# Performance work log

Measured on AMD Instinct MI355X. Metric: run time of the kernel, lower is better.

Reference implementation:

```python
import jax, jax.numpy as jnp
import numpy as np

B, L, D = 8, 2048, 2048
NH, HD = 32, 64          # num_heads, head_dim (D = NH*HD)
CS = 16                  # inner_net_chunk_size
BASE_LR = 1.0            # inner-loop base learning rate
EPS = 1e-6
ROPE_BASE = 10000.0


def setup_inputs() -> dict:
    key = jax.random.key(0)
    ks = jax.random.split(key, 6)
    s = 0.02
    return {
        "hidden_states": jax.random.normal(ks[0], (B, L, D), jnp.float32),
        "wq": jax.random.normal(ks[1], (D, D), jnp.float32) * s,
        "wk": jax.random.normal(ks[2], (D, D), jnp.float32) * s,
        "wv": jax.random.normal(ks[3], (D, D), jnp.float32) * s,
        "wo": jax.random.normal(ks[4], (D, D), jnp.float32) * s,
        "W1": jax.random.normal(ks[5], (NH, HD, HD), jnp.float32) * s,
        "b1": jnp.zeros((NH, 1, HD), jnp.float32),
        "ttt_norm_weight": jnp.ones((NH, HD), jnp.float32),
        "ttt_norm_bias": jnp.zeros((NH, HD), jnp.float32),
    }


def _rotate_half(x):
    x1, x2 = jnp.split(x, 2, axis=-1)
    return jnp.concatenate((-x2, x1), axis=-1)


def _permute_qk(x):
    b, h, l, f = x.shape
    return x.reshape(b, h, l, f // 2, 2).transpose(0, 1, 2, 4, 3).reshape(b, h, l, f)


def _undo_permute_qk(x):
    b, h, l, f = x.shape
    return x.reshape(b, h, l, 2, f // 2).transpose(0, 1, 2, 4, 3).reshape(b, h, l, f)


def _ln_fwd(x, g, b):
    mu = x.mean(-1, keepdims=True)
    var = ((x - mu) ** 2).mean(-1, keepdims=True)
    xh = (x - mu) * jax.lax.rsqrt(var + EPS)
    return g * xh + b


def _ln_fused_l2_bwd(x, target, g, b):
    # grad of 0.5*||LN(x) - target||^2 w.r.t. x, fused (TTT inner-loop loss grad)
    f = x.shape[-1]
    mu = x.mean(-1, keepdims=True)
    var = ((x - mu) ** 2).mean(-1, keepdims=True)
    std = jnp.sqrt(var + EPS)
    xh = (x - mu) / std
    gout = (g * xh + b) - target
    gxh = gout * g
    return (f * gxh - gxh.sum(-1, keepdims=True)
            - xh * (gxh * xh).sum(-1, keepdims=True)) / (f * std)


def reference(hidden_states, wq, wk, wv, wo, W1, b1, ttt_norm_weight, ttt_norm_bias):
    Bx, Lx, Dx = hidden_states.shape
    nc = Lx // CS

    def proj(w):  # [B,L,D] -> [B,NH,L,HD]
        return (hidden_states @ w).reshape(Bx, Lx, NH, HD).transpose(0, 2, 1, 3)

    XQ, XK, XV = proj(wq), proj(wk), proj(wv)

    # rotary embedding (with permute/undo as in the source)
    inv_freq = 1.0 / (ROPE_BASE ** (jnp.arange(0, HD, 2, dtype=jnp.float32) / HD))
    freqs = jnp.outer(jnp.arange(Lx, dtype=jnp.float32), inv_freq)
    emb = jnp.concatenate((freqs, freqs), axis=-1)
    cos, sin = jnp.cos(emb)[None, None], jnp.sin(emb)[None, None]
    XQ, XK = _permute_qk(XQ), _permute_qk(XK)
    XQ = XQ * cos + _rotate_half(XQ) * sin
    XK = XK * cos + _rotate_half(XK) * sin
    XQ, XK = _undo_permute_qk(XQ), _undo_permute_qk(XK)

    def chunk(x):  # [B,NH,L,HD] -> [nc,B,NH,CS,HD]
        return x.reshape(Bx, NH, nc, CS, HD).transpose(2, 0, 1, 3, 4)

    XQc, XKc, XVc = chunk(XQ), chunk(XK), chunk(XV)

    g = ttt_norm_weight[None, :, None, :]   # [1,NH,1,HD]
    bb = ttt_norm_bias[None, :, None, :]

    token_idx = 1.0 / jnp.arange(1, CS + 1, dtype=jnp.float32)   # buffer from __init__
    eta = BASE_LR * token_idx                                    # [CS]
    tril_eta = jnp.tril(jnp.ones((CS, CS), jnp.float32)) * eta[:, None]
    last_eta = eta[-1]

    W1_0 = jnp.broadcast_to(W1[None], (Bx, NH, HD, HD))
    b1_0 = jnp.broadcast_to(b1[None], (Bx, NH, 1, HD))

    def step(carry, xs):
        W1s, b1s = carry
        xq, xk, xv = xs                                          # [B,NH,CS,HD]
        Z1 = jnp.einsum('bhkf,bhfg->bhkg', xk, W1s) + b1s
        grad = _ln_fused_l2_bwd(Z1, xv - xk, g, bb)              # dl/dZ1
        attn = jnp.tril(jnp.einsum('bhkf,bhlf->bhkl', xq, xk))   # causal within chunk
        b1_bar = b1s - jnp.einsum('kl,bhlf->bhkf', tril_eta, grad)
        Z1_bar = (jnp.einsum('bhkf,bhfg->bhkg', xq, W1s)
                  - jnp.einsum('bhkl,bhlf->bhkf', eta[None, None, :, None] * attn, grad)
                  + b1_bar)
        W1_new = W1s - last_eta * jnp.einsum('bhkf,bhkg->bhfg', xk, grad)
        b1_new = b1s - last_eta * grad.sum(-2, keepdims=True)
        out = xq + _ln_fwd(Z1_bar, g, bb)                        # residual + post-LN
        return (W1_new, b1_new), out

    _, outs = jax.lax.scan(step, (W1_0, b1_0), (XQc, XKc, XVc))  # [nc,B,NH,CS,HD]
    out = (outs.transpose(1, 2, 0, 3, 4).reshape(Bx, NH, Lx, HD)
               .transpose(0, 2, 1, 3).reshape(Bx, Lx, Dx))
    return out @ wo
```

## Files before the change

### kernel.cpp

```cpp
#include <hip/hip_runtime.h>

typedef __bf16 bf16;
typedef __bf16 bf16x4 __attribute__((ext_vector_type(4)));
typedef __bf16 bf16x8 __attribute__((ext_vector_type(8)));
typedef float floatx4 __attribute__((ext_vector_type(4)));

#define BB 8
#define LL 2048
#define DD 2048
#define NHH 32
#define HDD 64

#define MFMA16(a, b, c) __builtin_amdgcn_mfma_f32_16x16x32_bf16(a, b, c, 0, 0, 0)

__device__ __forceinline__ void gl_lds16(const void* g, void* l) {
  __builtin_amdgcn_global_load_lds((const __attribute__((address_space(1))) void*)g,
                                   (__attribute__((address_space(3))) void*)l, 16, 0, 0);
}

__global__ __launch_bounds__(256) void cast_bf16(const float* __restrict__ src,
                                                 bf16* __restrict__ dst)
{
  size_t i = ((size_t)blockIdx.x * 256 + threadIdx.x) * 8;
  floatx4 a = *(const floatx4*)(src + i);
  floatx4 b = *(const floatx4*)(src + i + 4);
  bf16x8 v;
  v[0] = (bf16)a[0]; v[1] = (bf16)a[1]; v[2] = (bf16)a[2]; v[3] = (bf16)a[3];
  v[4] = (bf16)b[0]; v[5] = (bf16)b[1]; v[6] = (bf16)b[2]; v[7] = (bf16)b[3];
  *(bf16x8*)(dst + i) = v;
}

__global__ __launch_bounds__(256) void transpose1(const float* __restrict__ src,
                                                  bf16* __restrict__ dst)
{
  __shared__ float tile[64][65];
  const int t = threadIdx.x;
  const int col = t & 63, rw = t >> 6;
  const int bx = blockIdx.x * 64, by = blockIdx.y * 64;
  for (int i = rw; i < 64; i += 4)
    tile[i][col] = src[(size_t)(by + i) * DD + bx + col];
  __syncthreads();
  for (int i = rw; i < 64; i += 4)
    dst[(size_t)(bx + i) * DD + by + col] = (bf16)tile[col][i];
}

template<int AIDX, int EPI>
__global__ __launch_bounds__(256) void gemm_bt(const bf16* __restrict__ Ab,
    const bf16* __restrict__ BT, void* __restrict__ Cv)
{
  constexpr int Kd = 2048;
  __shared__ alignas(16) bf16 As[128 * 64];
  __shared__ alignas(16) bf16 Bs[128 * 64];
  const int t = threadIdx.x;
  const int id = blockIdx.y * 16 + blockIdx.x;
  const int swz = (id & 7) * 256 + (id >> 3);
  const int bn = swz & 15, bm = swz >> 4;
  const int wave = t >> 6, lane = t & 63;
  const int m16 = lane & 15, quad = lane >> 4;
  floatx4 acc[2][8] = {};
  const int r0 = t >> 3;
  const int scc = (t & 7) ^ (r0 & 7);
  const bf16* Bb = BT + (size_t)(bn * 128) * Kd;
  char* AsB = (char*)As + wave * 1024;
  char* BsB = (char*)Bs + wave * 1024;

  for (int k0 = 0; k0 < Kd; k0 += 64) {
    for (int i = 0; i < 4; ++i) {
      int r = r0 + 32 * i;
      int col = k0 + scc * 8;
      const bf16* ga;
      if (AIDX == 0) {
        ga = Ab + (size_t)(bm * 128 + r) * Kd + col;
      } else {
        int R = bm * 128 + r;
        int b = R >> 11, l = R & 2047;
        int h = col >> 6, f = col & 63;
        ga = Ab + (((size_t)(b * NHH + h) * LL + l) * HDD + f);
      }
      gl_lds16(ga, AsB + i * 4096);
      gl_lds16(Bb + (size_t)r * Kd + col, BsB + i * 4096);
    }
    __syncthreads();
    const int sw = m16 & 7;
    for (int kk = 0; kk < 2; ++kk) {
      bf16x8 af[2], bfr[8];
      const int c = ((kk * 4 + quad) ^ sw) * 8;
      for (int mt = 0; mt < 2; ++mt)
        af[mt] = *(const bf16x8*)&As[(wave * 32 + mt * 16 + m16) * 64 + c];
      for (int nt = 0; nt < 8; ++nt)
        bfr[nt] = *(const bf16x8*)&Bs[(nt * 16 + m16) * 64 + c];
      for (int mt = 0; mt < 2; ++mt)
        for (int nt = 0; nt < 8; ++nt)
          acc[mt][nt] = MFMA16(af[mt], bfr[nt], acc[mt][nt]);
    }
    __syncthreads();
  }

  for (int mt = 0; mt < 2; ++mt)
    for (int nt = 0; nt < 8; ++nt)
      for (int rg = 0; rg < 4; ++rg) {
        int row = bm * 128 + wave * 32 + mt * 16 + quad * 4 + rg;
        int col = bn * 128 + nt * 16 + m16;
        if (EPI == 0) {
          ((float*)Cv)[(size_t)row * DD + col] = acc[mt][nt][rg];
        } else {
          int b = row >> 11, l = row & 2047;
          int h = col >> 6, f = col & 63;
          ((bf16*)Cv)[((size_t)(b * NHH + h) * LL + l) * HDD + f] = (bf16)acc[mt][nt][rg];
        }
      }
}

__global__ __launch_bounds__(256) void rope_qk(bf16* __restrict__ Q, bf16* __restrict__ Kt)
{
  bf16* X = blockIdx.y ? Kt : Q;
  unsigned p = blockIdx.x * 256u + threadIdx.x;
  int i = p & 31;
  int l = (p >> 5) & 2047;
  int bh = p >> 16;
  float invf = expf(-(float)i * 0.28782313662425573f);
  float th = (float)l * invf;
  float cs = cosf(th), sn = sinf(th);
  size_t off = (size_t)bh * (LL * HDD) + (size_t)l * HDD + 2 * i;
  float x0 = (float)X[off], x1 = (float)X[off + 1];
  X[off]     = (bf16)(x0 * cs - x1 * sn);
  X[off + 1] = (bf16)(x1 * cs + x0 * sn);
}

__global__ __launch_bounds__(256) void ttt_scan(
    const bf16* Q, const bf16* __restrict__ Kx,
    const bf16* __restrict__ V, const float* __restrict__ W1g,
    const float* __restrict__ b1g, const float* __restrict__ gw,
    const float* __restrict__ gb, bf16* O)
{
  const int bh = blockIdx.x, h = bh & 31;
  const int t = threadIdx.x;
  const int wave = t >> 6, lane = t & 63;
  const int q = lane >> 4, i16 = lane & 15;
  const int kr = t >> 4, sr = t & 15, f0 = sr * 4;

  __shared__ alignas(16) bf16 W1Th[64 * 72];
  __shared__ alignas(16) bf16 W1Tl[64 * 72];
  __shared__ alignas(16) bf16 xqs[2][16 * 72];
  __shared__ alignas(16) bf16 xks[2][16 * 72];
  __shared__ alignas(16) bf16 xvs[2][16 * 72];
  __shared__ alignas(16) bf16 xkTs[64 * 24];
  __shared__ alignas(16) bf16 gTh[64 * 24];
  __shared__ alignas(16) bf16 gTl[64 * 24];
  __shared__ alignas(16) bf16 Pm[16 * 24];
  __shared__ alignas(16) float Z1s[16 * 68];

  floatx4 accW[4];
  const float* Wg = W1g + (size_t)h * 4096;
  for (int mt = 0; mt < 4; ++mt)
    for (int r = 0; r < 4; ++r)
      accW[mt][r] = Wg[(16 * mt + 4 * q + r) * 64 + 16 * wave + i16];
  float b1r = b1g[h * 64 + 16 * wave + i16];

  for (int mt = 0; mt < 4; ++mt) {
    bf16x4 h4, l4;
    for (int r = 0; r < 4; ++r) {
      float w = accW[mt][r];
      bf16 hi = (bf16)w;
      h4[r] = hi; l4[r] = (bf16)(w - (float)hi);
    }
    int base = (16 * wave + i16) * 72 + 16 * mt + 4 * q;
    *(bf16x4*)&W1Th[base] = h4;
    *(bf16x4*)&W1Tl[base] = l4;
  }

  float gq[4], bq[4];
  for (int j = 0; j < 4; ++j) {
    gq[j] = gw[h * 64 + f0 + j];
    bq[j] = gb[h * 64 + f0 + j];
  }
  float etar[4];
  for (int r = 0; r < 4; ++r) etar[r] = 1.0f / (float)(4 * q + r + 1);

  const size_t qbase = (size_t)bh * (LL * HDD);
  bf16x4 rq = *(const bf16x4*)(Q  + qbase + kr * 64 + f0);
  bf16x4 rk = *(const bf16x4*)(Kx + qbase + kr * 64 + f0);
  bf16x4 rv = *(const bf16x4*)(V  + qbase + kr * 64 + f0);

  for (int c = 0; c < 128; ++c) {
    const int pb = c & 1;
    *(bf16x4*)&xqs[pb][kr * 72 + f0] = rq;
    *(bf16x4*)&xks[pb][kr * 72 + f0] = rk;
    *(bf16x4*)&xvs[pb][kr * 72 + f0] = rv;
    for (int j = 0; j < 4; ++j)
      xkTs[(f0 + j) * 24 + kr] = (bf16)((float)rk[j] * -0.0625f);
    __syncthreads();

    bf16x8 akf[2], whi[2], wlo[2];
    akf[0] = *(const bf16x8*)&xks[pb][i16 * 72 + q * 8];
    akf[1] = *(const bf16x8*)&xks[pb][i16 * 72 + 32 + q * 8];
    {
      int wb = (16 * wave + i16) * 72 + q * 8;
      whi[0] = *(const bf16x8*)&W1Th[wb];
      whi[1] = *(const bf16x8*)&W1Th[wb + 32];
      wlo[0] = *(const bf16x8*)&W1Tl[wb];
      wlo[1] = *(const bf16x8*)&W1Tl[wb + 32];
    }
    {
      floatx4 z = {b1r, b1r, b1r, b1r};
      z = MFMA16(akf[0], whi[0], z);
      z = MFMA16(akf[1], whi[1], z);
      z = MFMA16(akf[0], wlo[0], z);
      z = MFMA16(akf[1], wlo[1], z);
      for (int r = 0; r < 4; ++r)
        Z1s[(4 * q + r) * 68 + 16 * wave + i16] = z[r];
    }
    if (wave == 0) {
      bf16x8 aq0 = *(const bf16x8*)&xqs[pb][i16 * 72 + q * 8];
      bf16x8 aq1 = *(const bf16x8*)&xqs[pb][i16 * 72 + 32 + q * 8];
      floatx4 at = {};
      at = MFMA16(aq0, akf[0], at);
      at = MFMA16(aq1, akf[1], at);
      for (int r = 0; r < 4; ++r) {
        int krow = 4 * q + r;
        float pv = (i16 <= krow) ? -(at[r] + 1.0f) * etar[r] : 0.0f;
        Pm[krow * 24 + i16] = (bf16)pv;
      }
    }
    __syncthreads();

    {
      floatx4 z4 = *(const floatx4*)&Z1s[kr * 68 + f0];
      float tg[4], sum = 0.f, ssq = 0.f;
      for (int j = 0; j < 4; ++j) {
        tg[j] = (float)rv[j] - (float)rk[j];
        sum += z4[j]; ssq += z4[j] * z4[j];
      }
      for (int m = 1; m < 16; m <<= 1) { sum += __shfl_xor(sum, m, 64); ssq += __shfl_xor(ssq, m, 64); }
      float mu = sum * (1.f / 64.f);
      float var = ssq * (1.f / 64.f) - mu * mu;
      float rstd = rsqrtf(var + 1e-6f);
      float xh[4], gx[4], s1 = 0.f, s2 = 0.f;
      for (int j = 0; j < 4; ++j) {
        xh[j] = (z4[j] - mu) * rstd;
        float go = gq[j] * xh[j] + bq[j] - tg[j];
        gx[j] = go * gq[j];
        s1 += gx[j]; s2 += gx[j] * xh[j];
      }
      for (int m = 1; m < 16; m <<= 1) { s1 += __shfl_xor(s1, m, 64); s2 += __shfl_xor(s2, m, 64); }
      for (int j = 0; j < 4; ++j) {
        float gr = (64.f * gx[j] - s1 - xh[j] * s2) * (rstd * (1.f / 64.f));
        bf16 hi = (bf16)gr;
        gTh[(f0 + j) * 24 + kr] = hi;
        gTl[(f0 + j) * 24 + kr] = (bf16)(gr - (float)hi);
      }
    }
    __syncthreads();

    {
      const size_t cb = qbase + (size_t)(c + 1) * 1024 + kr * 64 + f0;
      rq = *(const bf16x4*)(Q  + cb);
      rk = *(const bf16x4*)(Kx + cb);
      rv = *(const bf16x4*)(V  + cb);
    }

    {
      bf16x8 aq0 = *(const bf16x8*)&xqs[pb][i16 * 72 + q * 8];
      bf16x8 aq1 = *(const bf16x8*)&xqs[pb][i16 * 72 + 32 + q * 8];
      bf16x8 pf  = *(const bf16x8*)&Pm[i16 * 24 + (q & 1) * 8];
      const bf16* gT = (q < 2) ? gTh : gTl;
      bf16x8 bgp = *(const bf16x8*)&gT[(16 * wave + i16) * 24 + (q & 1) * 8];
      floatx4 zb = {b1r, b1r, b1r, b1r};
      zb = MFMA16(aq0, whi[0], zb);
      zb = MFMA16(aq1, whi[1], zb);
      zb = MFMA16(aq0, wlo[0], zb);
      zb = MFMA16(aq1, wlo[1], zb);
      zb = MFMA16(pf, bgp, zb);
      for (int r = 0; r < 4; ++r)
        Z1s[(4 * q + r) * 68 + 16 * wave + i16] = zb[r];

      for (int mt = 0; mt < 4; ++mt) {
        bf16x8 axk = *(const bf16x8*)&xkTs[(16 * mt + i16) * 24 + (q & 1) * 8];
        accW[mt] = MFMA16(axk, bgp, accW[mt]);
      }
      for (int mt = 0; mt < 4; ++mt) {
        bf16x4 h4, l4;
        for (int r = 0; r < 4; ++r) {
          float w = accW[mt][r];
          bf16 hi = (bf16)w;
          h4[r] = hi; l4[r] = (bf16)(w - (float)hi);
        }
        int base = (16 * wave + i16) * 72 + 16 * mt + 4 * q;
        *(bf16x4*)&W1Th[base] = h4;
        *(bf16x4*)&W1Tl[base] = l4;
      }
      {
        const bf16* rh = &gTh[(16 * wave + i16) * 24];
        const bf16* rl = &gTl[(16 * wave + i16) * 24];
        bf16x8 a0 = *(const bf16x8*)rh, a1 = *(const bf16x8*)(rh + 8);
        bf16x8 a2 = *(const bf16x8*)rl, a3 = *(const bf16x8*)(rl + 8);
        float s = 0.f;
        for (int j = 0; j < 8; ++j)
          s += (float)a0[j] + (float)a1[j] + (float)a2[j] + (float)a3[j];
        b1r -= 0.0625f * s;
      }
    }
    __syncthreads();

    {
      floatx4 z4 = *(const floatx4*)&Z1s[kr * 68 + f0];
      float sum = 0.f, ssq = 0.f;
      for (int j = 0; j < 4; ++j) { sum += z4[j]; ssq += z4[j] * z4[j]; }
      for (int m = 1; m < 16; m <<= 1) { sum += __shfl_xor(sum, m, 64); ssq += __shfl_xor(ssq, m, 64); }
      float mu = sum * (1.f / 64.f);
      float var = ssq * (1.f / 64.f) - mu * mu;
      float rstd = rsqrtf(var + 1e-6f);
      bf16x4 xq4 = *(const bf16x4*)&xqs[pb][kr * 72 + f0];
      bf16x4 o4;
      for (int j = 0; j < 4; ++j)
        o4[j] = (bf16)((float)xq4[j] + gq[j] * ((z4[j] - mu) * rstd) + bq[j]);
      *(bf16x4*)(O + qbase + (size_t)c * 1024 + kr * 64 + f0) = o4;
    }
  }
}

extern "C" void kernel_launch(void* const* d_in, const int* in_sizes, int n_in,
                              void* d_out, int out_size, void* d_ws, size_t ws_size,
                              hipStream_t stream)
{
  const float* X  = (const float*)d_in[0];
  const float* wq = (const float*)d_in[1];
  const float* wk = (const float*)d_in[2];
  const float* wv = (const float*)d_in[3];
  const float* wo = (const float*)d_in[4];
  const float* W1 = (const float*)d_in[5];
  const float* b1 = (const float*)d_in[6];
  const float* gw = (const float*)d_in[7];
  const float* gb = (const float*)d_in[8];

  bf16* ws = (bf16*)d_ws;
  const size_t NEl = (size_t)BB * LL * DD;
  bf16* Qb = ws;
  bf16* Kb = ws + NEl;
  bf16* WT = ws + 2 * NEl;
  bf16* Vb = (bf16*)d_out;
  bf16* Xb = (bf16*)d_out + NEl;

  cast_bf16<<<dim3(16384), 256, 0, stream>>>(X, Xb);
  transpose1<<<dim3(32, 32), 256, 0, stream>>>(wq, WT);
  gemm_bt<0, 1><<<dim3(16, 128), 256, 0, stream>>>(Xb, WT, Qb);
  transpose1<<<dim3(32, 32), 256, 0, stream>>>(wk, WT);
  gemm_bt<0, 1><<<dim3(16, 128), 256, 0, stream>>>(Xb, WT, Kb);
  transpose1<<<dim3(32, 32), 256, 0, stream>>>(wv, WT);
  gemm_bt<0, 1><<<dim3(16, 128), 256, 0, stream>>>(Xb, WT, Vb);
  rope_qk<<<dim3(65536, 2), 256, 0, stream>>>(Qb, Kb);
  ttt_scan<<<dim3(256), 256, 0, stream>>>(Qb, Kb, Vb, W1, b1, gw, gb, Qb);
  transpose1<<<dim3(32, 32), 256, 0, stream>>>(wo, WT);
  gemm_bt<1, 0><<<dim3(16, 128), 256, 0, stream>>>(Qb, WT, d_out);
}
```

Measured before the change: 1.209 ms.

## Pipeline GEMM with triple-buffered LDS, 256x128 tiles and 8 waves

Result: slower. 1.313 ms (+8.6%).

```diff
diff --git a/kernel.cpp b/kernel.cpp
--- a/kernel.cpp
+++ b/kernel.cpp
@@ -45,62 +45,100 @@
 }
 
 template<int AIDX, int EPI>
-__global__ __launch_bounds__(256) void gemm_bt(const bf16* __restrict__ Ab,
+__global__ __launch_bounds__(512) void gemm_bt(const bf16* __restrict__ Ab,
     const bf16* __restrict__ BT, void* __restrict__ Cv)
 {
   constexpr int Kd = 2048;
-  __shared__ alignas(16) bf16 As[128 * 64];
-  __shared__ alignas(16) bf16 Bs[128 * 64];
+  constexpr int NT = Kd / 64;
+  __shared__ alignas(16) bf16 As[3][256 * 64];
+  __shared__ alignas(16) bf16 Bs[3][128 * 64];
   const int t = threadIdx.x;
   const int id = blockIdx.y * 16 + blockIdx.x;
-  const int swz = (id & 7) * 256 + (id >> 3);
+  const int swz = (id & 7) * 128 + (id >> 3);
   const int bn = swz & 15, bm = swz >> 4;
-  const int wave = t >> 6, lane = t & 63;
-  const int m16 = lane & 15, quad = lane >> 4;
-  floatx4 acc[2][8] = {};
-  const int r0 = t >> 3;
-  const int scc = (t & 7) ^ (r0 & 7);
-  const bf16* Bb = BT + (size_t)(bn * 128) * Kd;
-  char* AsB = (char*)As + wave * 1024;
-  char* BsB = (char*)Bs + wave * 1024;
-
-  for (int k0 = 0; k0 < Kd; k0 += 64) {
-    for (int i = 0; i < 4; ++i) {
-      int r = r0 + 32 * i;
-      int col = k0 + scc * 8;
-      const bf16* ga;
-      if (AIDX == 0) {
-        ga = Ab + (size_t)(bm * 128 + r) * Kd + col;
-      } else {
-        int R = bm * 128 + r;
-        int b = R >> 11, l = R & 2047;
-        int h = col >> 6, f = col & 63;
-        ga = Ab + (((size_t)(b * NHH + h) * LL + l) * HDD + f);
-      }
-      gl_lds16(ga, AsB + i * 4096);
-      gl_lds16(Bb + (size_t)r * Kd + col, BsB + i * 4096);
-    }
-    __syncthreads();
-    const int sw = m16 & 7;
+  const int wv = t >> 6, ln = t & 63;
+  const int q = ln >> 4, i16 = ln & 15;
+  const int wm = wv >> 1, wn = wv & 1;
+  const int rsub = ln >> 3, csub = ln & 7;
+
+  floatx4 acc[4][4] = {};
+
+  size_t aoff[4], boff[2];
+#pragma unroll
+  for (int j = 0; j < 4; ++j) {
+    int r = (wv * 4 + j) * 8 + rsub;
+    int sc = (csub ^ (r & 7)) * 8;
+    if (AIDX == 0) {
+      aoff[j] = (size_t)(bm * 256 + r) * Kd + sc;
+    } else {
+      int R = bm * 256 + r;
+      int b = R >> 11, l = R & 2047;
+      aoff[j] = ((size_t)b * NHH * LL + l) * HDD + sc;
+    }
+  }
+#pragma unroll
+  for (int j = 0; j < 2; ++j) {
+    int r = (wv * 2 + j) * 8 + rsub;
+    int sc = (csub ^ (r & 7)) * 8;
+    boff[j] = (size_t)(bn * 128 + r) * Kd + sc;
+  }
+
+  auto STAGE = [&](int bi, int kt) {
+    char* abase = (char*)&As[bi][0] + wv * 4096;
+    char* bbase = (char*)&Bs[bi][0] + wv * 2048;
+#pragma unroll
+    for (int j = 0; j < 4; ++j) {
+      const bf16* ga = (AIDX == 0) ? (Ab + aoff[j] + kt * 64)
+                                   : (Ab + aoff[j] + (size_t)kt * (LL * HDD));
+      gl_lds16(ga, abase + j * 1024);
+    }
+#pragma unroll
+    for (int j = 0; j < 2; ++j)
+      gl_lds16(BT + boff[j] + kt * 64, bbase + j * 1024);
+  };
+
+  STAGE(0, 0);
+  STAGE(1, 1);
+  asm volatile("s_waitcnt vmcnt(6)\n\ts_barrier" ::: "memory");
+
+  int cur = 0;
+  for (int kt = 0; kt < NT; ++kt) {
+    int nxt = cur + 2; if (nxt >= 3) nxt -= 3;
+    int pf = kt + 2; if (pf >= NT) pf -= NT;
+    STAGE(nxt, pf);
+#pragma unroll
     for (int kk = 0; kk < 2; ++kk) {
-      bf16x8 af[2], bfr[8];
-      const int c = ((kk * 4 + quad) ^ sw) * 8;
-      for (int mt = 0; mt < 2; ++mt)
-        af[mt] = *(const bf16x8*)&As[(wave * 32 + mt * 16 + m16) * 64 + c];
-      for (int nt = 0; nt < 8; ++nt)
-        bfr[nt] = *(const bf16x8*)&Bs[(nt * 16 + m16) * 64 + c];
-      for (int mt = 0; mt < 2; ++mt)
-        for (int nt = 0; nt < 8; ++nt)
+      bf16x8 af[4], bfr[4];
+#pragma unroll
+      for (int mt = 0; mt < 4; ++mt) {
+        int r = wm * 64 + mt * 16 + i16;
+        int ch = ((kk * 4 + q) ^ (r & 7)) * 8;
+        af[mt] = *(const bf16x8*)&As[cur][r * 64 + ch];
+      }
+#pragma unroll
+      for (int nt = 0; nt < 4; ++nt) {
+        int r = wn * 64 + nt * 16 + i16;
+        int ch = ((kk * 4 + q) ^ (r & 7)) * 8;
+        bfr[nt] = *(const bf16x8*)&Bs[cur][r * 64 + ch];
+      }
+#pragma unroll
+      for (int mt = 0; mt < 4; ++mt)
+#pragma unroll
+        for (int nt = 0; nt < 4; ++nt)
           acc[mt][nt] = MFMA16(af[mt], bfr[nt], acc[mt][nt]);
     }
-    __syncthreads();
-  }
-
-  for (int mt = 0; mt < 2; ++mt)
-    for (int nt = 0; nt < 8; ++nt)
+    asm volatile("s_waitcnt vmcnt(6)\n\ts_barrier" ::: "memory");
+    cur = (cur + 1 == 3) ? 0 : cur + 1;
+  }
+
+#pragma unroll
+  for (int mt = 0; mt < 4; ++mt)
+#pragma unroll
+    for (int nt = 0; nt < 4; ++nt)
+#pragma unroll
       for (int rg = 0; rg < 4; ++rg) {
-        int row = bm * 128 + wave * 32 + mt * 16 + quad * 4 + rg;
-        int col = bn * 128 + nt * 16 + m16;
+        int row = bm * 256 + wm * 64 + mt * 16 + q * 4 + rg;
+        int col = bn * 128 + wn * 64 + nt * 16 + i16;
         if (EPI == 0) {
           ((float*)Cv)[(size_t)row * DD + col] = acc[mt][nt][rg];
         } else {
@@ -118,9 +156,10 @@
   int i = p & 31;
   int l = (p >> 5) & 2047;
   int bh = p >> 16;
-  float invf = expf(-(float)i * 0.28782313662425573f);
+  float invf = __expf(-(float)i * 0.28782313662425573f);
   float th = (float)l * invf;
-  float cs = cosf(th), sn = sinf(th);
+  float sn, cs;
+  __sincosf(th, &sn, &cs);
   size_t off = (size_t)bh * (LL * HDD) + (size_t)l * HDD + 2 * i;
   float x0 = (float)X[off], x1 = (float)X[off + 1];
   X[off]     = (bf16)(x0 * cs - x1 * sn);
@@ -343,13 +382,13 @@
 
   cast_bf16<<<dim3(16384), 256, 0, stream>>>(X, Xb);
   transpose1<<<dim3(32, 32), 256, 0, stream>>>(wq, WT);
-  gemm_bt<0, 1><<<dim3(16, 128), 256, 0, stream>>>(Xb, WT, Qb);
+  gemm_bt<0, 1><<<dim3(16, 64), 512, 0, stream>>>(Xb, WT, Qb);
   transpose1<<<dim3(32, 32), 256, 0, stream>>>(wk, WT);
-  gemm_bt<0, 1><<<dim3(16, 128), 256, 0, stream>>>(Xb, WT, Kb);
+  gemm_bt<0, 1><<<dim3(16, 64), 512, 0, stream>>>(Xb, WT, Kb);
   transpose1<<<dim3(32, 32), 256, 0, stream>>>(wv, WT);
-  gemm_bt<0, 1><<<dim3(16, 128), 256, 0, stream>>>(Xb, WT, Vb);
+  gemm_bt<0, 1><<<dim3(16, 64), 512, 0, stream>>>(Xb, WT, Vb);
   rope_qk<<<dim3(65536, 2), 256, 0, stream>>>(Qb, Kb);
   ttt_scan<<<dim3(256), 256, 0, stream>>>(Qb, Kb, Vb, W1, b1, gw, gb, Qb);
   transpose1<<<dim3(32, 32), 256, 0, stream>>>(wo, WT);
-  gemm_bt<1, 0><<<dim3(16, 128), 256, 0, stream>>>(Qb, WT, d_out);
-}
+  gemm_bt<1, 0><<<dim3(16, 64), 512, 0, stream>>>(Qb, WT, d_out);
+}
```

## Split TTT scan block into W-update and Q-output warp groups

Applied to the files above, without the earlier changes.

New measurement: 1.230 ms. Within noise of the previous version (+1.8%).

```diff
diff --git a/kernel.cpp b/kernel.cpp
--- a/kernel.cpp
+++ b/kernel.cpp
@@ -118,16 +118,17 @@
   int i = p & 31;
   int l = (p >> 5) & 2047;
   int bh = p >> 16;
-  float invf = expf(-(float)i * 0.28782313662425573f);
+  float invf = __expf(-(float)i * 0.28782313662425573f);
   float th = (float)l * invf;
-  float cs = cosf(th), sn = sinf(th);
+  float sn, cs;
+  __sincosf(th, &sn, &cs);
   size_t off = (size_t)bh * (LL * HDD) + (size_t)l * HDD + 2 * i;
   float x0 = (float)X[off], x1 = (float)X[off + 1];
   X[off]     = (bf16)(x0 * cs - x1 * sn);
   X[off + 1] = (bf16)(x1 * cs + x0 * sn);
 }
 
-__global__ __launch_bounds__(256) void ttt_scan(
+__global__ __launch_bounds__(512) void ttt_scan(
     const bf16* Q, const bf16* __restrict__ Kx,
     const bf16* __restrict__ V, const float* __restrict__ W1g,
     const float* __restrict__ b1g, const float* __restrict__ gw,
@@ -135,15 +136,17 @@
 {
   const int bh = blockIdx.x, h = bh & 31;
   const int t = threadIdx.x;
-  const int wave = t >> 6, lane = t & 63;
+  const int lane = t & 63, wv = t >> 6;
   const int q = lane >> 4, i16 = lane & 15;
-  const int kr = t >> 4, sr = t & 15, f0 = sr * 4;
+  const bool isW = wv < 4;
+  const int wg = wv & 3;
+  const int tg = t & 255;
+  const int kr = tg >> 4, sr = tg & 15, f0 = sr * 4;
 
   __shared__ alignas(16) bf16 W1Th[64 * 72];
   __shared__ alignas(16) bf16 W1Tl[64 * 72];
   __shared__ alignas(16) bf16 xqs[2][16 * 72];
   __shared__ alignas(16) bf16 xks[2][16 * 72];
-  __shared__ alignas(16) bf16 xvs[2][16 * 72];
   __shared__ alignas(16) bf16 xkTs[64 * 24];
   __shared__ alignas(16) bf16 gTh[64 * 24];
   __shared__ alignas(16) bf16 gTl[64 * 24];
@@ -152,83 +155,98 @@
 
   floatx4 accW[4];
   const float* Wg = W1g + (size_t)h * 4096;
-  for (int mt = 0; mt < 4; ++mt)
-    for (int r = 0; r < 4; ++r)
-      accW[mt][r] = Wg[(16 * mt + 4 * q + r) * 64 + 16 * wave + i16];
-  float b1r = b1g[h * 64 + 16 * wave + i16];
-
-  for (int mt = 0; mt < 4; ++mt) {
-    bf16x4 h4, l4;
-    for (int r = 0; r < 4; ++r) {
-      float w = accW[mt][r];
-      bf16 hi = (bf16)w;
-      h4[r] = hi; l4[r] = (bf16)(w - (float)hi);
-    }
-    int base = (16 * wave + i16) * 72 + 16 * mt + 4 * q;
-    *(bf16x4*)&W1Th[base] = h4;
-    *(bf16x4*)&W1Tl[base] = l4;
-  }
-
-  float gq[4], bq[4];
+  float b1r = b1g[h * 64 + 16 * wg + i16];
+  if (isW) {
+    for (int mt = 0; mt < 4; ++mt)
+      for (int r = 0; r < 4; ++r)
+        accW[mt][r] = Wg[(16 * mt + 4 * q + r) * 64 + 16 * wg + i16];
+    for (int mt = 0; mt < 4; ++mt) {
+      bf16x4 h4, l4;
+      for (int r = 0; r < 4; ++r) {
+        float w = accW[mt][r];
+        bf16 hi = (bf16)w;
+        h4[r] = hi; l4[r] = (bf16)(w - (float)hi);
+      }
+      int base = (16 * wg + i16) * 72 + 16 * mt + 4 * q;
+      *(bf16x4*)&W1Th[base] = h4;
+      *(bf16x4*)&W1Tl[base] = l4;
+    }
+  }
+  float gq4[4], bq4[4];
   for (int j = 0; j < 4; ++j) {
-    gq[j] = gw[h * 64 + f0 + j];
-    bq[j] = gb[h * 64 + f0 + j];
+    gq4[j] = gw[h * 64 + f0 + j];
+    bq4[j] = gb[h * 64 + f0 + j];
   }
   float etar[4];
   for (int r = 0; r < 4; ++r) etar[r] = 1.0f / (float)(4 * q + r + 1);
 
   const size_t qbase = (size_t)bh * (LL * HDD);
-  bf16x4 rq = *(const bf16x4*)(Q  + qbase + kr * 64 + f0);
-  bf16x4 rk = *(const bf16x4*)(Kx + qbase + kr * 64 + f0);
-  bf16x4 rv = *(const bf16x4*)(V  + qbase + kr * 64 + f0);
+  bf16x4 rq{}, rk{}, rv{};
+  if (isW) {
+    rk = *(const bf16x4*)(Kx + qbase + kr * 64 + f0);
+    rv = *(const bf16x4*)(V  + qbase + kr * 64 + f0);
+  } else {
+    rq = *(const bf16x4*)(Q + qbase + kr * 64 + f0);
+  }
+  floatx4 zq{};
 
   for (int c = 0; c < 128; ++c) {
     const int pb = c & 1;
-    *(bf16x4*)&xqs[pb][kr * 72 + f0] = rq;
-    *(bf16x4*)&xks[pb][kr * 72 + f0] = rk;
-    *(bf16x4*)&xvs[pb][kr * 72 + f0] = rv;
-    for (int j = 0; j < 4; ++j)
-      xkTs[(f0 + j) * 24 + kr] = (bf16)((float)rk[j] * -0.0625f);
-    __syncthreads();
-
-    bf16x8 akf[2], whi[2], wlo[2];
-    akf[0] = *(const bf16x8*)&xks[pb][i16 * 72 + q * 8];
-    akf[1] = *(const bf16x8*)&xks[pb][i16 * 72 + 32 + q * 8];
+    if (isW) {
+      *(bf16x4*)&xks[pb][kr * 72 + f0] = rk;
+      for (int j = 0; j < 4; ++j)
+        xkTs[(f0 + j) * 24 + kr] = (bf16)((float)rk[j] * -0.0625f);
+    } else {
+      *(bf16x4*)&xqs[pb][kr * 72 + f0] = rq;
+    }
+    __syncthreads();
+
     {
-      int wb = (16 * wave + i16) * 72 + q * 8;
-      whi[0] = *(const bf16x8*)&W1Th[wb];
-      whi[1] = *(const bf16x8*)&W1Th[wb + 32];
-      wlo[0] = *(const bf16x8*)&W1Tl[wb];
-      wlo[1] = *(const bf16x8*)&W1Tl[wb + 32];
-    }
-    {
-      floatx4 z = {b1r, b1r, b1r, b1r};
-      z = MFMA16(akf[0], whi[0], z);
-      z = MFMA16(akf[1], whi[1], z);
-      z = MFMA16(akf[0], wlo[0], z);
-      z = MFMA16(akf[1], wlo[1], z);
-      for (int r = 0; r < 4; ++r)
-        Z1s[(4 * q + r) * 68 + 16 * wave + i16] = z[r];
-    }
-    if (wave == 0) {
-      bf16x8 aq0 = *(const bf16x8*)&xqs[pb][i16 * 72 + q * 8];
-      bf16x8 aq1 = *(const bf16x8*)&xqs[pb][i16 * 72 + 32 + q * 8];
-      floatx4 at = {};
-      at = MFMA16(aq0, akf[0], at);
-      at = MFMA16(aq1, akf[1], at);
-      for (int r = 0; r < 4; ++r) {
-        int krow = 4 * q + r;
-        float pv = (i16 <= krow) ? -(at[r] + 1.0f) * etar[r] : 0.0f;
-        Pm[krow * 24 + i16] = (bf16)pv;
-      }
-    }
-    __syncthreads();
-
-    {
+      int wb = (16 * wg + i16) * 72 + q * 8;
+      bf16x8 whi0 = *(const bf16x8*)&W1Th[wb];
+      bf16x8 whi1 = *(const bf16x8*)&W1Th[wb + 32];
+      bf16x8 wlo0 = *(const bf16x8*)&W1Tl[wb];
+      bf16x8 wlo1 = *(const bf16x8*)&W1Tl[wb + 32];
+      if (isW) {
+        bf16x8 ak0 = *(const bf16x8*)&xks[pb][i16 * 72 + q * 8];
+        bf16x8 ak1 = *(const bf16x8*)&xks[pb][i16 * 72 + 32 + q * 8];
+        floatx4 z = {b1r, b1r, b1r, b1r};
+        z = MFMA16(ak0, whi0, z);
+        z = MFMA16(ak1, whi1, z);
+        z = MFMA16(ak0, wlo0, z);
+        z = MFMA16(ak1, wlo1, z);
+        for (int r = 0; r < 4; ++r)
+          Z1s[(4 * q + r) * 68 + 16 * wg + i16] = z[r];
+      } else {
+        bf16x8 aq0 = *(const bf16x8*)&xqs[pb][i16 * 72 + q * 8];
+        bf16x8 aq1 = *(const bf16x8*)&xqs[pb][i16 * 72 + 32 + q * 8];
+        floatx4 z = {b1r, b1r, b1r, b1r};
+        z = MFMA16(aq0, whi0, z);
+        z = MFMA16(aq1, whi1, z);
+        z = MFMA16(aq0, wlo0, z);
+        z = MFMA16(aq1, wlo1, z);
+        zq = z;
+        if (wv == 4) {
+          bf16x8 ak0 = *(const bf16x8*)&xks[pb][i16 * 72 + q * 8];
+          bf16x8 ak1 = *(const bf16x8*)&xks[pb][i16 * 72 + 32 + q * 8];
+          floatx4 at = {};
+          at = MFMA16(aq0, ak0, at);
+          at = MFMA16(aq1, ak1, at);
+          for (int r = 0; r < 4; ++r) {
+            int krow = 4 * q + r;
+            float pv = (i16 <= krow) ? -(at[r] + 1.0f) * etar[r] : 0.0f;
+            Pm[krow * 24 + i16] = (bf16)pv;
+          }
+        }
+      }
+    }
+    __syncthreads();
+
+    if (isW) {
       floatx4 z4 = *(const floatx4*)&Z1s[kr * 68 + f0];
-      float tg[4], sum = 0.f, ssq = 0.f;
+      float tg4[4], sum = 0.f, ssq = 0.f;
       for (int j = 0; j < 4; ++j) {
-        tg[j] = (float)rv[j] - (float)rk[j];
+        tg4[j] = (float)rv[j] - (float)rk[j];
         sum += z4[j]; ssq += z4[j] * z4[j];
       }
       for (int m = 1; m < 16; m <<= 1) { sum += __shfl_xor(sum, m, 64); ssq += __shfl_xor(ssq, m, 64); }
@@ -238,8 +256,8 @@
       float xh[4], gx[4], s1 = 0.f, s2 = 0.f;
       for (int j = 0; j < 4; ++j) {
         xh[j] = (z4[j] - mu) * rstd;
-        float go = gq[j] * xh[j] + bq[j] - tg[j];
-        gx[j] = go * gq[j];
+        float go = gq4[j] * xh[j] + bq4[j] - tg4[j];
+        gx[j] = go * gq4[j];
         s1 += gx[j]; s2 += gx[j] * xh[j];
       }
       for (int m = 1; m < 16; m <<= 1) { s1 += __shfl_xor(s1, m, 64); s2 += __shfl_xor(s2, m, 64); }
@@ -249,35 +267,49 @@
         gTh[(f0 + j) * 24 + kr] = hi;
         gTl[(f0 + j) * 24 + kr] = (bf16)(gr - (float)hi);
       }
-    }
-    __syncthreads();
-
-    {
+    } else {
       const size_t cb = qbase + (size_t)(c + 1) * 1024 + kr * 64 + f0;
-      rq = *(const bf16x4*)(Q  + cb);
+      rq = *(const bf16x4*)(Q + cb);
+    }
+    __syncthreads();
+
+    if (isW) {
+      const size_t cb = qbase + (size_t)(c + 1) * 1024 + kr * 64 + f0;
       rk = *(const bf16x4*)(Kx + cb);
-      rv = *(const bf16x4*)(V  + cb);
-    }
-
-    {
-      bf16x8 aq0 = *(const bf16x8*)&xqs[pb][i16 * 72 + q * 8];
-      bf16x8 aq1 = *(const bf16x8*)&xqs[pb][i16 * 72 + 32 + q * 8];
-      bf16x8 pf  = *(const bf16x8*)&Pm[i16 * 24 + (q & 1) * 8];
+      rv = *(const bf16x4*)(V + cb);
       const bf16* gT = (q < 2) ? gTh : gTl;
-      bf16x8 bgp = *(const bf16x8*)&gT[(16 * wave + i16) * 24 + (q & 1) * 8];
-      floatx4 zb = {b1r, b1r, b1r, b1r};
-      zb = MFMA16(aq0, whi[0], zb);
-      zb = MFMA16(aq1, whi[1], zb);
-      zb = MFMA16(aq0, wlo[0], zb);
-      zb = MFMA16(aq1, wlo[1], zb);
-      zb = MFMA16(pf, bgp, zb);
-      for (int r = 0; r < 4; ++r)
-        Z1s[(4 * q + r) * 68 + 16 * wave + i16] = zb[r];
-
+      bf16x8 bgp = *(const bf16x8*)&gT[(16 * wg + i16) * 24 + (q & 1) * 8];
       for (int mt = 0; mt < 4; ++mt) {
         bf16x8 axk = *(const bf16x8*)&xkTs[(16 * mt + i16) * 24 + (q & 1) * 8];
         accW[mt] = MFMA16(axk, bgp, accW[mt]);
       }
+      const bf16* rh = &gTh[(16 * wg + i16) * 24];
+      const bf16* rl = &gTl[(16 * wg + i16) * 24];
+      bf16x8 a0 = *(const bf16x8*)rh, a1 = *(const bf16x8*)(rh + 8);
+      bf16x8 a2 = *(const bf16x8*)rl, a3 = *(const bf16x8*)(rl + 8);
+      float s = 0.f;
+      for (int j = 0; j < 8; ++j)
+        s += (float)a0[j] + (float)a1[j] + (float)a2[j] + (float)a3[j];
+      b1r -= 0.0625f * s;
+    } else {
+      bf16x8 pf = *(const bf16x8*)&Pm[i16 * 24 + (q & 1) * 8];
+      const bf16* gT = (q < 2) ? gTh : gTl;
+      bf16x8 bgp = *(const bf16x8*)&gT[(16 * wg + i16) * 24 + (q & 1) * 8];
+      floatx4 zb = MFMA16(pf, bgp, zq);
+      for (int r = 0; r < 4; ++r)
+        Z1s[(4 * q + r) * 68 + 16 * wg + i16] = zb[r];
+      const bf16* rh = &gTh[(16 * wg + i16) * 24];
+      const bf16* rl = &gTl[(16 * wg + i16) * 24];
+      bf16x8 a0 = *(const bf16x8*)rh, a1 = *(const bf16x8*)(rh + 8);
+      bf16x8 a2 = *(const bf16x8*)rl, a3 = *(const bf16x8*)(rl + 8);
+      float s = 0.f;
+      for (int j = 0; j < 8; ++j)
+        s += (float)a0[j] + (float)a1[j] + (float)a2[j] + (float)a3[j];
+      b1r -= 0.0625f * s;
+    }
+    __syncthreads();
+
+    if (isW) {
       for (int mt = 0; mt < 4; ++mt) {
         bf16x4 h4, l4;
         for (int r = 0; r < 4; ++r) {
@@ -285,24 +317,11 @@
           bf16 hi = (bf16)w;
           h4[r] = hi; l4[r] = (bf16)(w - (float)hi);
         }
-        int base = (16 * wave + i16) * 72 + 16 * mt + 4 * q;
+        int base = (16 * wg + i16) * 72 + 16 * mt + 4 * q;
         *(bf16x4*)&W1Th[base] = h4;
         *(bf16x4*)&W1Tl[base] = l4;
       }
-      {
-        const bf16* rh = &gTh[(16 * wave + i16) * 24];
-        const bf16* rl = &gTl[(16 * wave + i16) * 24];
-        bf16x8 a0 = *(const bf16x8*)rh, a1 = *(const bf16x8*)(rh + 8);
-        bf16x8 a2 = *(const bf16x8*)rl, a3 = *(const bf16x8*)(rl + 8);
-        float s = 0.f;
-        for (int j = 0; j < 8; ++j)
-          s += (float)a0[j] + (float)a1[j] + (float)a2[j] + (float)a3[j];
-        b1r -= 0.0625f * s;
-      }
-    }
-    __syncthreads();
-
-    {
+    } else {
       floatx4 z4 = *(const floatx4*)&Z1s[kr * 68 + f0];
       float sum = 0.f, ssq = 0.f;
       for (int j = 0; j < 4; ++j) { sum += z4[j]; ssq += z4[j] * z4[j]; }
@@ -313,7 +332,7 @@
       bf16x4 xq4 = *(const bf16x4*)&xqs[pb][kr * 72 + f0];
       bf16x4 o4;
       for (int j = 0; j < 4; ++j)
-        o4[j] = (bf16)((float)xq4[j] + gq[j] * ((z4[j] - mu) * rstd) + bq[j]);
+        o4[j] = (bf16)((float)xq4[j] + gq4[j] * ((z4[j] - mu) * rstd) + bq4[j]);
       *(bf16x4*)(O + qbase + (size_t)c * 1024 + kr * 64 + f0) = o4;
     }
   }
@@ -349,7 +368,7 @@
   transpose1<<<dim3(32, 32), 256, 0, stream>>>(wv, WT);
   gemm_bt<0, 1><<<dim3(16, 128), 256, 0, stream>>>(Xb, WT, Vb);
   rope_qk<<<dim3(65536, 2), 256, 0, stream>>>(Qb, Kb);
-  ttt_scan<<<dim3(256), 256, 0, stream>>>(Qb, Kb, Vb, W1, b1, gw, gb, Qb);
+  ttt_scan<<<dim3(256), 512, 0, stream>>>(Qb, Kb, Vb, W1, b1, gw, gb, Qb);
   transpose1<<<dim3(32, 32), 256, 0, stream>>>(wo, WT);
   gemm_bt<1, 0><<<dim3(16, 128), 256, 0, stream>>>(Qb, WT, d_out);
 }
```

## Fuse RoPE into QK projection GEMM epilogue and pack transposed LDS stores

Applied to the files above, without the earlier changes.

Measured after the change: 1.196 ms. Within noise of the previous version (-1.1%).

```diff
diff --git a/kernel.cpp b/kernel.cpp
--- a/kernel.cpp
+++ b/kernel.cpp
@@ -16,6 +16,10 @@
 __device__ __forceinline__ void gl_lds16(const void* g, void* l) {
   __builtin_amdgcn_global_load_lds((const __attribute__((address_space(1))) void*)g,
                                    (__attribute__((address_space(3))) void*)l, 16, 0, 0);
+}
+
+__device__ __forceinline__ unsigned bfbits(bf16 x) {
+  union { bf16 b; unsigned short u; } c; c.b = x; return (unsigned)c.u;
 }
 
 __global__ __launch_bounds__(256) void cast_bf16(const float* __restrict__ src,
@@ -44,7 +48,7 @@
     dst[(size_t)(bx + i) * DD + by + col] = (bf16)tile[col][i];
 }
 
-template<int AIDX, int EPI>
+template<int AIDX, int EPI, int RP>
 __global__ __launch_bounds__(256) void gemm_bt(const bf16* __restrict__ Ab,
     const bf16* __restrict__ BT, void* __restrict__ Cv)
 {
@@ -96,35 +100,36 @@
     __syncthreads();
   }
 
+  float invf[8];
+  if (RP) {
+#pragma unroll
+    for (int nt = 0; nt < 8; ++nt) {
+      int col = bn * 128 + nt * 16 + m16;
+      int i = (col >> 1) & 31;
+      invf[nt] = __expf(-(float)i * 0.28782313662425573f);
+    }
+  }
+
   for (int mt = 0; mt < 2; ++mt)
     for (int nt = 0; nt < 8; ++nt)
       for (int rg = 0; rg < 4; ++rg) {
         int row = bm * 128 + wave * 32 + mt * 16 + quad * 4 + rg;
         int col = bn * 128 + nt * 16 + m16;
+        float v = acc[mt][nt][rg];
+        if (RP) {
+          float o = __shfl_xor(v, 1, 64);
+          float sn, cs;
+          __sincosf((float)(row & 2047) * invf[nt], &sn, &cs);
+          v = (m16 & 1) ? (v * cs + o * sn) : (v * cs - o * sn);
+        }
         if (EPI == 0) {
-          ((float*)Cv)[(size_t)row * DD + col] = acc[mt][nt][rg];
+          ((float*)Cv)[(size_t)row * DD + col] = v;
         } else {
           int b = row >> 11, l = row & 2047;
           int h = col >> 6, f = col & 63;
-          ((bf16*)Cv)[((size_t)(b * NHH + h) * LL + l) * HDD + f] = (bf16)acc[mt][nt][rg];
+          ((bf16*)Cv)[((size_t)(b * NHH + h) * LL + l) * HDD + f] = (bf16)v;
         }
       }
-}
-
-__global__ __launch_bounds__(256) void rope_qk(bf16* __restrict__ Q, bf16* __restrict__ Kt)
-{
-  bf16* X = blockIdx.y ? Kt : Q;
-  unsigned p = blockIdx.x * 256u + threadIdx.x;
-  int i = p & 31;
-  int l = (p >> 5) & 2047;
-  int bh = p >> 16;
-  float invf = expf(-(float)i * 0.28782313662425573f);
-  float th = (float)l * invf;
-  float cs = cosf(th), sn = sinf(th);
-  size_t off = (size_t)bh * (LL * HDD) + (size_t)l * HDD + 2 * i;
-  float x0 = (float)X[off], x1 = (float)X[off + 1];
-  X[off]     = (bf16)(x0 * cs - x1 * sn);
-  X[off + 1] = (bf16)(x1 * cs + x0 * sn);
 }
 
 __global__ __launch_bounds__(256) void ttt_scan(
@@ -143,7 +148,6 @@
   __shared__ alignas(16) bf16 W1Tl[64 * 72];
   __shared__ alignas(16) bf16 xqs[2][16 * 72];
   __shared__ alignas(16) bf16 xks[2][16 * 72];
-  __shared__ alignas(16) bf16 xvs[2][16 * 72];
   __shared__ alignas(16) bf16 xkTs[64 * 24];
   __shared__ alignas(16) bf16 gTh[64 * 24];
   __shared__ alignas(16) bf16 gTl[64 * 24];
@@ -186,9 +190,20 @@
     const int pb = c & 1;
     *(bf16x4*)&xqs[pb][kr * 72 + f0] = rq;
     *(bf16x4*)&xks[pb][kr * 72 + f0] = rk;
-    *(bf16x4*)&xvs[pb][kr * 72 + f0] = rv;
-    for (int j = 0; j < 4; ++j)
-      xkTs[(f0 + j) * 24 + kr] = (bf16)((float)rk[j] * -0.0625f);
+    {
+      bf16 s0 = (bf16)((float)rk[0] * -0.0625f), s1 = (bf16)((float)rk[1] * -0.0625f);
+      bf16 s2 = (bf16)((float)rk[2] * -0.0625f), s3 = (bf16)((float)rk[3] * -0.0625f);
+      unsigned p0 = bfbits(s0) | (bfbits(s1) << 16);
+      unsigned p1 = bfbits(s2) | (bfbits(s3) << 16);
+      unsigned q0 = (unsigned)__shfl_xor((int)p0, 16, 64);
+      unsigned q1 = (unsigned)__shfl_xor((int)p1, 16, 64);
+      if (!(kr & 1)) {
+        *(unsigned*)&xkTs[(f0 + 0) * 24 + kr] = (p0 & 0xffffu) | (q0 << 16);
+        *(unsigned*)&xkTs[(f0 + 1) * 24 + kr] = (p0 >> 16) | (q0 & 0xffff0000u);
+        *(unsigned*)&xkTs[(f0 + 2) * 24 + kr] = (p1 & 0xffffu) | (q1 << 16);
+        *(unsigned*)&xkTs[(f0 + 3) * 24 + kr] = (p1 >> 16) | (q1 & 0xffff0000u);
+      }
+    }
     __syncthreads();
 
     bf16x8 akf[2], whi[2], wlo[2];
@@ -243,11 +258,32 @@
         s1 += gx[j]; s2 += gx[j] * xh[j];
       }
       for (int m = 1; m < 16; m <<= 1) { s1 += __shfl_xor(s1, m, 64); s2 += __shfl_xor(s2, m, 64); }
-      for (int j = 0; j < 4; ++j) {
-        float gr = (64.f * gx[j] - s1 - xh[j] * s2) * (rstd * (1.f / 64.f));
-        bf16 hi = (bf16)gr;
-        gTh[(f0 + j) * 24 + kr] = hi;
-        gTl[(f0 + j) * 24 + kr] = (bf16)(gr - (float)hi);
+      unsigned hp0, hp1, lp0, lp1;
+      {
+        bf16 hb[4], lb[4];
+        for (int j = 0; j < 4; ++j) {
+          float gr = (64.f * gx[j] - s1 - xh[j] * s2) * (rstd * (1.f / 64.f));
+          hb[j] = (bf16)gr;
+          lb[j] = (bf16)(gr - (float)hb[j]);
+        }
+        hp0 = bfbits(hb[0]) | (bfbits(hb[1]) << 16);
+        hp1 = bfbits(hb[2]) | (bfbits(hb[3]) << 16);
+        lp0 = bfbits(lb[0]) | (bfbits(lb[1]) << 16);
+        lp1 = bfbits(lb[2]) | (bfbits(lb[3]) << 16);
+      }
+      unsigned qh0 = (unsigned)__shfl_xor((int)hp0, 16, 64);
+      unsigned qh1 = (unsigned)__shfl_xor((int)hp1, 16, 64);
+      unsigned ql0 = (unsigned)__shfl_xor((int)lp0, 16, 64);
+      unsigned ql1 = (unsigned)__shfl_xor((int)lp1, 16, 64);
+      if (!(kr & 1)) {
+        *(unsigned*)&gTh[(f0 + 0) * 24 + kr] = (hp0 & 0xffffu) | (qh0 << 16);
+        *(unsigned*)&gTh[(f0 + 1) * 24 + kr] = (hp0 >> 16) | (qh0 & 0xffff0000u);
+        *(unsigned*)&gTh[(f0 + 2) * 24 + kr] = (hp1 & 0xffffu) | (qh1 << 16);
+        *(unsigned*)&gTh[(f0 + 3) * 24 + kr] = (hp1 >> 16) | (qh1 & 0xffff0000u);
+        *(unsigned*)&gTl[(f0 + 0) * 24 + kr] = (lp0 & 0xffffu) | (ql0 << 16);
+        *(unsigned*)&gTl[(f0 + 1) * 24 + kr] = (lp0 >> 16) | (ql0 & 0xffff0000u);
+        *(unsigned*)&gTl[(f0 + 2) * 24 + kr] = (lp1 & 0xffffu) | (ql1 << 16);
+        *(unsigned*)&gTl[(f0 + 3) * 24 + kr] = (lp1 >> 16) | (ql1 & 0xffff0000u);
       }
     }
     __syncthreads();
@@ -343,13 +379,12 @@
 
   cast_bf16<<<dim3(16384), 256, 0, stream>>>(X, Xb);
   transpose1<<<dim3(32, 32), 256, 0, stream>>>(wq, WT);
-  gemm_bt<0, 1><<<dim3(16, 128), 256, 0, stream>>>(Xb, WT, Qb);
+  gemm_bt<0, 1, 1><<<dim3(16, 128), 256, 0, stream>>>(Xb, WT, Qb);
   transpose1<<<dim3(32, 32), 256, 0, stream>>>(wk, WT);
-  gemm_bt<0, 1><<<dim3(16, 128), 256, 0, stream>>>(Xb, WT, Kb);
+  gemm_bt<0, 1, 1><<<dim3(16, 128), 256, 0, stream>>>(Xb, WT, Kb);
   transpose1<<<dim3(32, 32), 256, 0, stream>>>(wv, WT);
-  gemm_bt<0, 1><<<dim3(16, 128), 256, 0, stream>>>(Xb, WT, Vb);
-  rope_qk<<<dim3(65536, 2), 256, 0, stream>>>(Qb, Kb);
+  gemm_bt<0, 1, 0><<<dim3(16, 128), 256, 0, stream>>>(Xb, WT, Vb);
   ttt_scan<<<dim3(256), 256, 0, stream>>>(Qb, Kb, Vb, W1, b1, gw, gb, Qb);
   transpose1<<<dim3(32, 32), 256, 0, stream>>>(wo, WT);
-  gemm_bt<1, 0><<<dim3(16, 128), 256, 0, stream>>>(Qb, WT, d_out);
-}
+  gemm_bt<1, 0, 0><<<dim3(16, 128), 256, 0, stream>>>(Qb, WT, d_out);
+}
```
